# Optimization experiments

Hardware: AMD Instinct MI355X
Metric: run time of the kernel (lower is better)

## Reference

```python
import jax, jax.numpy as jnp
import numpy as np

N_NODES = 100000
N_EDGES = 1600000
IN_DIM = 512
HID = 64
OUT_DIM = 5


def _gcn_conv(x, row, col, w, W, b, n_nodes):
    """PyG GCNConv: h = x @ W; out[col] += norm * h[row]; out += b.
    norm = deg^-1/2[row] * w * deg^-1/2[col], deg from edge weights scattered on col,
    with self-loops (weight 1) already appended by caller."""
    h = x @ W  # [N, F_out]
    deg = jax.ops.segment_sum(w, col, num_segments=n_nodes)  # [N]
    dinv = jnp.where(deg > 0, jax.lax.rsqrt(deg), 0.0)
    norm = dinv[row] * w * dinv[col]  # [E']
    msg = h[row] * norm[:, None]  # [E', F_out] edge-wise gather + scale
    out = jax.ops.segment_sum(msg, col, num_segments=n_nodes)  # scatter-add
    return out + b


def setup_inputs() -> dict:
    key = jax.random.key(0)
    ks = jax.random.split(key, 10)
    x = jax.random.normal(ks[0], (N_NODES, IN_DIM), dtype=jnp.float32)
    edge_index = jax.random.randint(ks[1], (2, N_EDGES), 0, N_NODES, dtype=jnp.int32)
    edge_attr = jax.random.uniform(ks[2], (N_EDGES,), dtype=jnp.float32)
    # Glorot-ish init for params
    W1 = jax.random.normal(ks[3], (IN_DIM, HID), dtype=jnp.float32) * (1.0 / np.sqrt(IN_DIM))
    b1 = jnp.zeros((HID,), dtype=jnp.float32)
    W2 = jax.random.normal(ks[4], (HID, HID), dtype=jnp.float32) * (1.0 / np.sqrt(HID))
    b2 = jnp.zeros((HID,), dtype=jnp.float32)
    Wfc = jax.random.normal(ks[5], (HID, OUT_DIM), dtype=jnp.float32) * (1.0 / np.sqrt(HID))
    bfc = jnp.zeros((OUT_DIM,), dtype=jnp.float32)
    return {"x": x, "edge_index": edge_index, "edge_attr": edge_attr,
            "W1": W1, "b1": b1, "W2": W2, "b2": b2, "Wfc": Wfc, "bfc": bfc}


def reference(x, edge_index, edge_attr, W1, b1, W2, b2, Wfc, bfc):
    n = x.shape[0]
    loop = jnp.arange(n, dtype=edge_index.dtype)
    row = jnp.concatenate([edge_index[0], loop])  # source nodes + self-loops
    col = jnp.concatenate([edge_index[1], loop])  # target nodes + self-loops
    w = jnp.concatenate([edge_attr, jnp.ones((n,), dtype=edge_attr.dtype)])
    h = jax.nn.relu(_gcn_conv(x, row, col, w, W1, b1, n))
    # dropout(p=0.5) is identity in eval/reference mode
    h = jax.nn.relu(_gcn_conv(h, row, col, w, W2, b2, n))
    return h @ Wfc + bfc
```

## Files before the change

kernel.cpp:

```cpp
#include <hip/hip_runtime.h>

#define HID 64
#define OUTD 5
#define BCAP 16384
#define PART_CHUNK 4096

typedef __attribute__((ext_vector_type(8))) short bf16x8;
typedef __attribute__((ext_vector_type(4))) float f32x4;

__device__ inline void split_bf16(float x, short& hi, short& lo) {
    unsigned u = __float_as_uint(x);
    unsigned h = u >> 16;
    float hf = __uint_as_float(h << 16);
    float lof = x - hf;
    unsigned l = __float_as_uint(lof) >> 16;
    hi = (short)h; lo = (short)l;
}

__device__ inline ushort f2bf(float x) {
    unsigned u = __float_as_uint(x);
    u += 0x7fffu + ((u >> 16) & 1u);
    return (ushort)(u >> 16);
}
__device__ inline float bf2f(ushort b) {
    return __uint_as_float(((unsigned)b) << 16);
}

__global__ void k_prep(const float* __restrict__ W1, const float* __restrict__ W2,
                       short* __restrict__ w1hi, short* __restrict__ w1lo,
                       short* __restrict__ w2hi, short* __restrict__ w2lo,
                       int* __restrict__ gcursor, int nbuck) {
    int gid = blockIdx.x * blockDim.x + threadIdx.x;
    if (gid < nbuck) gcursor[gid] = 0;
    if (gid >= 32768 + 4096) return;
    int which = (gid >= 32768);
    int g = which ? gid - 32768 : gid;
    const float* W = which ? W2 : W1;
    short* ph = which ? w2hi : w1hi;
    short* pl = which ? w2lo : w1lo;
    int b = g & 7, lane = (g >> 3) & 63, c = (g >> 9) & 3, s = g >> 11;
    int k = s * 32 + 8 * (lane >> 4) + b;
    int j = c * 16 + (lane & 15);
    float x = W[k * 64 + j];
    short hi, lo; split_bf16(x, hi, lo);
    ph[g] = hi; pl[g] = lo;
}

template<int K>
__device__ inline void gemm_body(const float* __restrict__ A,
                                 const short* __restrict__ whi,
                                 const short* __restrict__ wlo,
                                 ushort* __restrict__ C, int M, int bid, int tid) {
    const int NS = K / 32;
    int lane = tid & 63;
    int wave = tid >> 6;
    int r0 = bid * 128 + wave * 32;

    int ar0 = r0 + (lane & 15);      if (ar0 >= M) ar0 = M - 1;
    int ar1 = r0 + 16 + (lane & 15); if (ar1 >= M) ar1 = M - 1;
    const float* pa0 = A + (size_t)ar0 * K + 8 * (lane >> 4);
    const float* pa1 = A + (size_t)ar1 * K + 8 * (lane >> 4);
    const bf16x8* bh = (const bf16x8*)whi + lane;
    const bf16x8* bl = (const bf16x8*)wlo + lane;

    f32x4 acc[2][4];
    #pragma unroll
    for (int r = 0; r < 2; r++)
        #pragma unroll
        for (int c = 0; c < 4; c++) acc[r][c] = (f32x4){0.f, 0.f, 0.f, 0.f};

    #pragma unroll
    for (int s = 0; s < NS; s++) {
        float4 x0 = *(const float4*)(pa0 + s * 32);
        float4 x1 = *(const float4*)(pa0 + s * 32 + 4);
        float4 y0 = *(const float4*)(pa1 + s * 32);
        float4 y1 = *(const float4*)(pa1 + s * 32 + 4);
        float xs[8] = {x0.x, x0.y, x0.z, x0.w, x1.x, x1.y, x1.z, x1.w};
        float ys[8] = {y0.x, y0.y, y0.z, y0.w, y1.x, y1.y, y1.z, y1.w};
        bf16x8 ah0, al0, ah1, al1;
        #pragma unroll
        for (int e = 0; e < 8; e++) {
            short h, l;
            split_bf16(xs[e], h, l); ah0[e] = h; al0[e] = l;
            split_bf16(ys[e], h, l); ah1[e] = h; al1[e] = l;
        }
        #pragma unroll
        for (int c = 0; c < 4; c++) {
            bf16x8 wh = bh[(s * 4 + c) * 64];
            bf16x8 wl = bl[(s * 4 + c) * 64];
            acc[0][c] = __builtin_amdgcn_mfma_f32_16x16x32_bf16(ah0, wh, acc[0][c], 0, 0, 0);
            acc[0][c] = __builtin_amdgcn_mfma_f32_16x16x32_bf16(ah0, wl, acc[0][c], 0, 0, 0);
            acc[0][c] = __builtin_amdgcn_mfma_f32_16x16x32_bf16(al0, wh, acc[0][c], 0, 0, 0);
            acc[1][c] = __builtin_amdgcn_mfma_f32_16x16x32_bf16(ah1, wh, acc[1][c], 0, 0, 0);
            acc[1][c] = __builtin_amdgcn_mfma_f32_16x16x32_bf16(ah1, wl, acc[1][c], 0, 0, 0);
            acc[1][c] = __builtin_amdgcn_mfma_f32_16x16x32_bf16(al1, wh, acc[1][c], 0, 0, 0);
        }
    }

    #pragma unroll
    for (int r = 0; r < 2; r++) {
        #pragma unroll
        for (int reg = 0; reg < 4; reg++) {
            int grow = r0 + r * 16 + 4 * (lane >> 4) + reg;
            if (grow < M) {
                #pragma unroll
                for (int c = 0; c < 4; c++)
                    C[(size_t)grow * 64 + c * 16 + (lane & 15)] = f2bf(acc[r][c][reg]);
            }
        }
    }
}

__global__ __launch_bounds__(256) void k_fused1(const float* __restrict__ x,
                                                const short* __restrict__ w1hi,
                                                const short* __restrict__ w1lo,
                                                ushort* __restrict__ h1, int M, int gGemm,
                                                const int* __restrict__ row,
                                                const int* __restrict__ col,
                                                const float* __restrict__ ea,
                                                int* __restrict__ gcursor,
                                                int2* __restrict__ bucket_mem,
                                                int nbuck, int E) {
    __shared__ int sh[512];
    int bid = blockIdx.x;
    int t = threadIdx.x;
    if (bid < gGemm) {
        gemm_body<512>(x, w1hi, w1lo, h1, M, bid, t);
        return;
    }
    int* hist = sh;
    int* basearr = sh + 256;
    int pb = bid - gGemm;
    int e0 = pb * PART_CHUNK;
    if (t < nbuck) hist[t] = 0;
    __syncthreads();
    int cols[PART_CHUNK / 256];
    #pragma unroll
    for (int i = 0; i < PART_CHUNK / 256; i++) {
        int e = e0 + t + i * 256;
        cols[i] = (e < E) ? col[e] : -1;
        if (cols[i] >= 0) atomicAdd(&hist[cols[i] >> 9], 1);
    }
    __syncthreads();
    if (t < nbuck) {
        basearr[t] = atomicAdd(&gcursor[t], hist[t]);
        hist[t] = 0;
    }
    __syncthreads();
    #pragma unroll
    for (int i = 0; i < PART_CHUNK / 256; i++) {
        int e = e0 + t + i * 256;
        if (e < E) {
            int c = cols[i];
            int b = c >> 9;
            int pos = basearr[b] + atomicAdd(&hist[b], 1);
            if (pos < BCAP) {
                int pack = ((c & 511) << 17) | row[e];
                bucket_mem[(size_t)b * BCAP + pos] = make_int2(pack, __float_as_int(ea[e]));
            }
        }
    }
}

__global__ __launch_bounds__(256) void k_build(const int* __restrict__ gcursor,
                                               const int2* __restrict__ bucket_mem,
                                               int2* __restrict__ edges,
                                               int2* __restrict__ nodemeta,
                                               float* __restrict__ dinv, int n) {
    __shared__ int hcnt[512];
    __shared__ int hoff[512];
    __shared__ float hdeg[512];
    __shared__ int ps[256];
    int b = blockIdx.x;
    int t = threadIdx.x;
    int cntb = gcursor[b]; if (cntb > BCAP) cntb = BCAP;
    const int2* bm = bucket_mem + (size_t)b * BCAP;

    #pragma unroll
    for (int l = t; l < 512; l += 256) { hcnt[l] = 0; hdeg[l] = 0.f; }
    __syncthreads();
    for (int i = t; i < cntb; i += 256) atomicAdd(&hcnt[bm[i].x >> 17], 1);
    __syncthreads();
    int c0 = hcnt[2 * t], c1 = hcnt[2 * t + 1];
    int q0 = (c0 + 15) & ~15, q1 = (c1 + 15) & ~15;
    ps[t] = q0 + q1;
    __syncthreads();
    for (int o = 1; o < 256; o <<= 1) {
        int v = (t >= o) ? ps[t - o] : 0;
        __syncthreads();
        ps[t] += v;
        __syncthreads();
    }
    int excl = ps[t] - (q0 + q1);
    hoff[2 * t] = excl;
    hoff[2 * t + 1] = excl + q0;
    __syncthreads();
    #pragma unroll
    for (int l = t; l < 512; l += 256) hcnt[l] = 0;
    __syncthreads();
    for (int i = t; i < cntb; i += 256) {
        int2 eM = bm[i];
        int local = eM.x >> 17;
        int src = eM.x & 0x1FFFF;
        int p = hoff[local] + atomicAdd(&hcnt[local], 1);
        edges[(size_t)b * BCAP + p] = make_int2(src, eM.y);
        atomicAdd(&hdeg[local], __int_as_float(eM.y));
    }
    __syncthreads();
    #pragma unroll
    for (int l = t; l < 512; l += 256) {
        int node = b * 512 + l;
        if (node < n) {
            int cnt = hcnt[l];
            int pc = (cnt + 15) & ~15;
            for (int p2 = cnt; p2 < pc; p2++)
                edges[(size_t)b * BCAP + hoff[l] + p2] = make_int2(node, 0);
            nodemeta[node] = make_int2(b * BCAP + hoff[l], pc);
            dinv[node] = rsqrtf(hdeg[l] + 1.0f);
        }
    }
}

__global__ void k_norm(const int2* __restrict__ nodemeta, int2* __restrict__ edges,
                       const float* __restrict__ dinv, int n) {
    int gw = (blockIdx.x * blockDim.x + threadIdx.x) >> 6;
    int lane = threadIdx.x & 63;
    if (gw >= n) return;
    int2 meta = nodemeta[gw];
    int2* seg = edges + meta.x;
    for (int i = lane; i < meta.y; i += 64) {
        int2 c = seg[i];
        c.y = __float_as_int(dinv[c.x] * __int_as_float(c.y));
        seg[i] = c;
    }
}

template<int FC>
__global__ void k_gather(const ushort* __restrict__ h, const int2* __restrict__ nodemeta,
                         const int2* __restrict__ edges, const float* __restrict__ dinv,
                         const float* __restrict__ bias, const float* __restrict__ Wfc,
                         const float* __restrict__ bfc, float* __restrict__ out, int n) {
    int gw = (blockIdx.x * blockDim.x + threadIdx.x) >> 6;
    int lane = threadIdx.x & 63;
    if (gw >= n) return;
    int2 meta = nodemeta[gw];
    int cnt = meta.y;
    const int2* seg = edges + meta.x;
    float self = bf2f(h[(size_t)gw * 64 + lane]);
    float dvc = dinv[gw];
    float acc = 0.f;

    if (cnt == 16) {
        int4 p[8];
        #pragma unroll
        for (int q = 0; q < 8; q++) p[q] = *(const int4*)(seg + 2 * q);
        float v[16];
        #pragma unroll
        for (int q = 0; q < 8; q++) {
            v[2 * q]     = bf2f(h[(size_t)p[q].x * 64 + lane]);
            v[2 * q + 1] = bf2f(h[(size_t)p[q].z * 64 + lane]);
        }
        #pragma unroll
        for (int q = 0; q < 8; q++)
            acc += __int_as_float(p[q].y) * v[2 * q] + __int_as_float(p[q].w) * v[2 * q + 1];
    } else if (cnt == 32) {
        int4 pA[8], pB[8];
        #pragma unroll
        for (int q = 0; q < 8; q++) pA[q] = *(const int4*)(seg + 2 * q);
        #pragma unroll
        for (int q = 0; q < 8; q++) pB[q] = *(const int4*)(seg + 16 + 2 * q);
        float vA[16], vB[16];
        #pragma unroll
        for (int q = 0; q < 8; q++) {
            vA[2 * q]     = bf2f(h[(size_t)pA[q].x * 64 + lane]);
            vA[2 * q + 1] = bf2f(h[(size_t)pA[q].z * 64 + lane]);
        }
        #pragma unroll
        for (int q = 0; q < 8; q++) {
            vB[2 * q]     = bf2f(h[(size_t)pB[q].x * 64 + lane]);
            vB[2 * q + 1] = bf2f(h[(size_t)pB[q].z * 64 + lane]);
        }
        #pragma unroll
        for (int q = 0; q < 8; q++)
            acc += __int_as_float(pA[q].y) * vA[2 * q] + __int_as_float(pA[q].w) * vA[2 * q + 1];
        #pragma unroll
        for (int q = 0; q < 8; q++)
            acc += __int_as_float(pB[q].y) * vB[2 * q] + __int_as_float(pB[q].w) * vB[2 * q + 1];
    } else {
        for (int i = 0; i < cnt; i += 16) {
            int4 p[8];
            #pragma unroll
            for (int q = 0; q < 8; q++) p[q] = *(const int4*)(seg + i + 2 * q);
            float v[16];
            #pragma unroll
            for (int q = 0; q < 8; q++) {
                v[2 * q]     = bf2f(h[(size_t)p[q].x * 64 + lane]);
                v[2 * q + 1] = bf2f(h[(size_t)p[q].z * 64 + lane]);
            }
            #pragma unroll
            for (int q = 0; q < 8; q++)
                acc += __int_as_float(p[q].y) * v[2 * q] + __int_as_float(p[q].w) * v[2 * q + 1];
        }
    }

    acc = dvc * acc + dvc * dvc * self + bias[lane];
    acc = fmaxf(acc, 0.f);
    if (FC == 0) {
        out[(size_t)gw * 64 + lane] = acc;
    } else {
        float res = 0.f;
        #pragma unroll
        for (int j = 0; j < OUTD; j++) {
            float p = acc * Wfc[lane * OUTD + j];
            #pragma unroll
            for (int o = 1; o < 64; o <<= 1) p += __shfl_xor(p, o);
            if (lane == j) res = p;
        }
        if (lane < OUTD) out[(size_t)gw * OUTD + lane] = res + bfc[lane];
    }
}

__global__ __launch_bounds__(256) void k_gemm2(const float* __restrict__ A,
                                               const short* __restrict__ whi,
                                               const short* __restrict__ wlo,
                                               ushort* __restrict__ C, int M) {
    gemm_body<64>(A, whi, wlo, C, M, blockIdx.x, threadIdx.x);
}

extern "C" void kernel_launch(void* const* d_in, const int* in_sizes, int n_in,
                              void* d_out, int out_size, void* d_ws, size_t ws_size,
                              hipStream_t stream) {
    const float* x   = (const float*)d_in[0];
    const int*   ei  = (const int*)d_in[1];
    const float* ea  = (const float*)d_in[2];
    const float* W1  = (const float*)d_in[3];
    const float* b1  = (const float*)d_in[4];
    const float* W2  = (const float*)d_in[5];
    const float* b2  = (const float*)d_in[6];
    const float* Wfc = (const float*)d_in[7];
    const float* bfc = (const float*)d_in[8];

    const int N = in_sizes[0] / 512;
    const int E = in_sizes[1] / 2;
    const int nbuck = (N + 511) >> 9;

    const int* row = ei;
    const int* col = ei + E;

    uintptr_t p = (uintptr_t)d_ws;
    auto carve = [&](size_t bytes) -> void* {
        void* r = (void*)p;
        p += (bytes + 255) & ~(size_t)255;
        return r;
    };
    int*    gcursor    = (int*)carve((size_t)nbuck * 4);
    float*  dinv       = (float*)carve((size_t)N * 4);
    int2*   nodemeta   = (int2*)carve((size_t)N * 8);
    int2*   bucket_mem = (int2*)carve((size_t)nbuck * BCAP * 8);
    int2*   edges      = (int2*)carve((size_t)nbuck * BCAP * 8);
    short*  w1hi       = (short*)carve(32768 * 2);
    short*  w1lo       = (short*)carve(32768 * 2);
    short*  w2hi       = (short*)carve(4096 * 2);
    short*  w2lo       = (short*)carve(4096 * 2);
    ushort* hbuf       = (ushort*)carve((size_t)N * 64 * 2);
    float*  gbuf       = (float*)carve((size_t)N * 64 * 4);
    (void)ws_size;

    const int B = 256;
    int gGemm = (N + 127) / 128;
    int gPart = (E + PART_CHUNK - 1) / PART_CHUNK;
    int gWave = (N * 64 + B - 1) / B;
    int gPrep = (32768 + 4096 + B - 1) / B;

    k_prep<<<gPrep, B, 0, stream>>>(W1, W2, w1hi, w1lo, w2hi, w2lo, gcursor, nbuck);
    k_fused1<<<gGemm + gPart, B, 0, stream>>>(x, w1hi, w1lo, hbuf, N, gGemm,
                                              row, col, ea, gcursor, bucket_mem, nbuck, E);
    k_build<<<nbuck, B, 0, stream>>>(gcursor, bucket_mem, edges, nodemeta, dinv, N);
    k_norm<<<gWave, B, 0, stream>>>(nodemeta, edges, dinv, N);
    k_gather<0><<<gWave, B, 0, stream>>>(hbuf, nodemeta, edges, dinv, b1,
                                         nullptr, nullptr, gbuf, N);
    k_gemm2<<<gGemm, B, 0, stream>>>(gbuf, w2hi, w2lo, hbuf, N);
    k_gather<1><<<gWave, B, 0, stream>>>(hbuf, nodemeta, edges, dinv, b2,
                                         Wfc, bfc, (float*)d_out, N);
}
```

Baseline: 282.6 us.

## Process two nodes per wave in gather and store layer-1 output as bf16

The gather kernel now assigns two nodes per wavefront, with each lane loading two packed bf16 features as one 32-bit word. This halves the wave count and raises bytes per load. The intermediate activation after layer 1 is stored as bf16 instead of fp32, and the second GEMM reads bf16 directly, which halves that buffer's traffic but adds rounding error on layer-1 outputs. Every node segment is padded to at least 16 entries so the unified loop can always load full 16-edge chunks, at the cost of some wasted padding work.

```diff
diff --git a/kernel.cpp b/kernel.cpp
--- a/kernel.cpp
+++ b/kernel.cpp
@@ -46,12 +46,11 @@
     ph[g] = hi; pl[g] = lo;
 }
 
-template<int K>
-__device__ inline void gemm_body(const float* __restrict__ A,
-                                 const short* __restrict__ whi,
-                                 const short* __restrict__ wlo,
-                                 ushort* __restrict__ C, int M, int bid, int tid) {
-    const int NS = K / 32;
+__device__ inline void gemm1_body(const float* __restrict__ A,
+                                  const short* __restrict__ whi,
+                                  const short* __restrict__ wlo,
+                                  ushort* __restrict__ C, int M, int bid, int tid) {
+    const int K = 512, NS = 16;
     int lane = tid & 63;
     int wave = tid >> 6;
     int r0 = bid * 128 + wave * 32;
@@ -125,7 +124,7 @@
     int bid = blockIdx.x;
     int t = threadIdx.x;
     if (bid < gGemm) {
-        gemm_body<512>(x, w1hi, w1lo, h1, M, bid, t);
+        gemm1_body(x, w1hi, w1lo, h1, M, bid, t);
         return;
     }
     int* hist = sh;
@@ -182,7 +181,8 @@
     for (int i = t; i < cntb; i += 256) atomicAdd(&hcnt[bm[i].x >> 17], 1);
     __syncthreads();
     int c0 = hcnt[2 * t], c1 = hcnt[2 * t + 1];
-    int q0 = (c0 + 15) & ~15, q1 = (c1 + 15) & ~15;
+    int q0 = (c0 + 15) & ~15; if (q0 < 16) q0 = 16;
+    int q1 = (c1 + 15) & ~15; if (q1 < 16) q1 = 16;
     ps[t] = q0 + q1;
     __syncthreads();
     for (int o = 1; o < 256; o <<= 1) {
@@ -212,7 +212,7 @@
         int node = b * 512 + l;
         if (node < n) {
             int cnt = hcnt[l];
-            int pc = (cnt + 15) & ~15;
+            int pc = (cnt + 15) & ~15; if (pc < 16) pc = 16;
             for (int p2 = cnt; p2 < pc; p2++)
                 edges[(size_t)b * BCAP + hoff[l] + p2] = make_int2(node, 0);
             nodemeta[node] = make_int2(b * BCAP + hoff[l], pc);
@@ -236,95 +236,123 @@
 }
 
 template<int FC>
-__global__ void k_gather(const ushort* __restrict__ h, const int2* __restrict__ nodemeta,
-                         const int2* __restrict__ edges, const float* __restrict__ dinv,
-                         const float* __restrict__ bias, const float* __restrict__ Wfc,
-                         const float* __restrict__ bfc, float* __restrict__ out, int n) {
+__global__ void k_gather2(const ushort* __restrict__ h, const int2* __restrict__ nodemeta,
+                          const int2* __restrict__ edges, const float* __restrict__ dinv,
+                          const float* __restrict__ bias, const float* __restrict__ Wfc,
+                          const float* __restrict__ bfc, ushort* __restrict__ outb,
+                          float* __restrict__ outf, int n) {
     int gw = (blockIdx.x * blockDim.x + threadIdx.x) >> 6;
     int lane = threadIdx.x & 63;
-    if (gw >= n) return;
-    int2 meta = nodemeta[gw];
+    int half = lane >> 5;
+    int s = lane & 31;
+    int node = gw * 2 + half;
+    bool valid = (node < n);
+    if (node >= n) node = n - 1;
+
+    int2 meta = nodemeta[node];
     int cnt = meta.y;
     const int2* seg = edges + meta.x;
-    float self = bf2f(h[(size_t)gw * 64 + lane]);
-    float dvc = dinv[gw];
-    float acc = 0.f;
-
-    if (cnt == 16) {
-        int4 p[8];
-        #pragma unroll
-        for (int q = 0; q < 8; q++) p[q] = *(const int4*)(seg + 2 * q);
-        float v[16];
+    uint self_u = *(const uint*)&h[(size_t)node * 64 + 2 * s];
+    float dvc = dinv[node];
+    int othercnt = __shfl_xor(cnt, 32);
+    int maxcnt = max(cnt, othercnt);
+
+    float acc0 = 0.f, acc1 = 0.f;
+    for (int i = 0; i < maxcnt; i += 16) {
+        int base = (i < cnt) ? i : (cnt - 16);
+        float live = (i < cnt) ? 1.f : 0.f;
+        int4 m[8];
+        #pragma unroll
+        for (int q = 0; q < 8; q++) m[q] = *(const int4*)(seg + base + 2 * q);
+        uint v[16];
         #pragma unroll
         for (int q = 0; q < 8; q++) {
-            v[2 * q]     = bf2f(h[(size_t)p[q].x * 64 + lane]);
-            v[2 * q + 1] = bf2f(h[(size_t)p[q].z * 64 + lane]);
-        }
-        #pragma unroll
-        for (int q = 0; q < 8; q++)
-            acc += __int_as_float(p[q].y) * v[2 * q] + __int_as_float(p[q].w) * v[2 * q + 1];
-    } else if (cnt == 32) {
-        int4 pA[8], pB[8];
-        #pragma unroll
-        for (int q = 0; q < 8; q++) pA[q] = *(const int4*)(seg + 2 * q);
-        #pragma unroll
-        for (int q = 0; q < 8; q++) pB[q] = *(const int4*)(seg + 16 + 2 * q);
-        float vA[16], vB[16];
+            v[2 * q]     = *(const uint*)&h[(size_t)m[q].x * 64 + 2 * s];
+            v[2 * q + 1] = *(const uint*)&h[(size_t)m[q].z * 64 + 2 * s];
+        }
         #pragma unroll
         for (int q = 0; q < 8; q++) {
-            vA[2 * q]     = bf2f(h[(size_t)pA[q].x * 64 + lane]);
-            vA[2 * q + 1] = bf2f(h[(size_t)pA[q].z * 64 + lane]);
-        }
-        #pragma unroll
-        for (int q = 0; q < 8; q++) {
-            vB[2 * q]     = bf2f(h[(size_t)pB[q].x * 64 + lane]);
-            vB[2 * q + 1] = bf2f(h[(size_t)pB[q].z * 64 + lane]);
-        }
-        #pragma unroll
-        for (int q = 0; q < 8; q++)
-            acc += __int_as_float(pA[q].y) * vA[2 * q] + __int_as_float(pA[q].w) * vA[2 * q + 1];
-        #pragma unroll
-        for (int q = 0; q < 8; q++)
-            acc += __int_as_float(pB[q].y) * vB[2 * q] + __int_as_float(pB[q].w) * vB[2 * q + 1];
+            float w0 = __int_as_float(m[q].y) * live;
+            float w1 = __int_as_float(m[q].w) * live;
+            uint va = v[2 * q], vb = v[2 * q + 1];
+            acc0 += w0 * __uint_as_float(va << 16);
+            acc1 += w0 * __uint_as_float(va & 0xffff0000u);
+            acc0 += w1 * __uint_as_float(vb << 16);
+            acc1 += w1 * __uint_as_float(vb & 0xffff0000u);
+        }
+    }
+
+    float2 bv = *(const float2*)&bias[2 * s];
+    float sf0 = __uint_as_float(self_u << 16);
+    float sf1 = __uint_as_float(self_u & 0xffff0000u);
+    float r0 = fmaxf(dvc * acc0 + dvc * dvc * sf0 + bv.x, 0.f);
+    float r1 = fmaxf(dvc * acc1 + dvc * dvc * sf1 + bv.y, 0.f);
+
+    if (FC == 0) {
+        if (valid) {
+            uint o = ((uint)f2bf(r1) << 16) | (uint)f2bf(r0);
+            *(uint*)&outb[(size_t)node * 64 + 2 * s] = o;
+        }
     } else {
-        for (int i = 0; i < cnt; i += 16) {
-            int4 p[8];
+        #pragma unroll
+        for (int j = 0; j < OUTD; j++) {
+            float p = r0 * Wfc[(2 * s) * OUTD + j] + r1 * Wfc[(2 * s + 1) * OUTD + j];
             #pragma unroll
-            for (int q = 0; q < 8; q++) p[q] = *(const int4*)(seg + i + 2 * q);
-            float v[16];
-            #pragma unroll
-            for (int q = 0; q < 8; q++) {
-                v[2 * q]     = bf2f(h[(size_t)p[q].x * 64 + lane]);
-                v[2 * q + 1] = bf2f(h[(size_t)p[q].z * 64 + lane]);
-            }
-            #pragma unroll
-            for (int q = 0; q < 8; q++)
-                acc += __int_as_float(p[q].y) * v[2 * q] + __int_as_float(p[q].w) * v[2 * q + 1];
-        }
-    }
-
-    acc = dvc * acc + dvc * dvc * self + bias[lane];
-    acc = fmaxf(acc, 0.f);
-    if (FC == 0) {
-        out[(size_t)gw * 64 + lane] = acc;
-    } else {
-        float res = 0.f;
-        #pragma unroll
-        for (int j = 0; j < OUTD; j++) {
-            float p = acc * Wfc[lane * OUTD + j];
-            #pragma unroll
-            for (int o = 1; o < 64; o <<= 1) p += __shfl_xor(p, o);
-            if (lane == j) res = p;
-        }
-        if (lane < OUTD) out[(size_t)gw * OUTD + lane] = res + bfc[lane];
-    }
-}
-
-__global__ __launch_bounds__(256) void k_gemm2(const float* __restrict__ A,
+            for (int o = 1; o <= 16; o <<= 1) p += __shfl_xor(p, o);
+            if (s == j && valid) outf[(size_t)node * OUTD + j] = p + bfc[j];
+        }
+    }
+}
+
+__global__ __launch_bounds__(256) void k_gemm2(const ushort* __restrict__ A,
                                                const short* __restrict__ whi,
                                                const short* __restrict__ wlo,
                                                ushort* __restrict__ C, int M) {
-    gemm_body<64>(A, whi, wlo, C, M, blockIdx.x, threadIdx.x);
+    int tid = threadIdx.x;
+    int lane = tid & 63;
+    int wave = tid >> 6;
+    int r0 = blockIdx.x * 128 + wave * 32;
+
+    int ar0 = r0 + (lane & 15);      if (ar0 >= M) ar0 = M - 1;
+    int ar1 = r0 + 16 + (lane & 15); if (ar1 >= M) ar1 = M - 1;
+    const ushort* pa0 = A + (size_t)ar0 * 64 + 8 * (lane >> 4);
+    const ushort* pa1 = A + (size_t)ar1 * 64 + 8 * (lane >> 4);
+    const bf16x8* bh = (const bf16x8*)whi + lane;
+    const bf16x8* bl = (const bf16x8*)wlo + lane;
+
+    f32x4 acc[2][4];
+    #pragma unroll
+    for (int r = 0; r < 2; r++)
+        #pragma unroll
+        for (int c = 0; c < 4; c++) acc[r][c] = (f32x4){0.f, 0.f, 0.f, 0.f};
+
+    #pragma unroll
+    for (int s = 0; s < 2; s++) {
+        bf16x8 a0 = *(const bf16x8*)(pa0 + s * 32);
+        bf16x8 a1 = *(const bf16x8*)(pa1 + s * 32);
+        #pragma unroll
+        for (int c = 0; c < 4; c++) {
+            bf16x8 wh = bh[(s * 4 + c) * 64];
+            bf16x8 wl = bl[(s * 4 + c) * 64];
+            acc[0][c] = __builtin_amdgcn_mfma_f32_16x16x32_bf16(a0, wh, acc[0][c], 0, 0, 0);
+            acc[0][c] = __builtin_amdgcn_mfma_f32_16x16x32_bf16(a0, wl, acc[0][c], 0, 0, 0);
+            acc[1][c] = __builtin_amdgcn_mfma_f32_16x16x32_bf16(a1, wh, acc[1][c], 0, 0, 0);
+            acc[1][c] = __builtin_amdgcn_mfma_f32_16x16x32_bf16(a1, wl, acc[1][c], 0, 0, 0);
+        }
+    }
+
+    #pragma unroll
+    for (int r = 0; r < 2; r++) {
+        #pragma unroll
+        for (int reg = 0; reg < 4; reg++) {
+            int grow = r0 + r * 16 + 4 * (lane >> 4) + reg;
+            if (grow < M) {
+                #pragma unroll
+                for (int c = 0; c < 4; c++)
+                    C[(size_t)grow * 64 + c * 16 + (lane & 15)] = f2bf(acc[r][c][reg]);
+            }
+        }
+    }
 }
 
 extern "C" void kernel_launch(void* const* d_in, const int* in_sizes, int n_in,
@@ -363,23 +391,24 @@
     short*  w2hi       = (short*)carve(4096 * 2);
     short*  w2lo       = (short*)carve(4096 * 2);
     ushort* hbuf       = (ushort*)carve((size_t)N * 64 * 2);
-    float*  gbuf       = (float*)carve((size_t)N * 64 * 4);
+    ushort* abuf       = (ushort*)carve((size_t)N * 64 * 2);
     (void)ws_size;
 
     const int B = 256;
-    int gGemm = (N + 127) / 128;
-    int gPart = (E + PART_CHUNK - 1) / PART_CHUNK;
-    int gWave = (N * 64 + B - 1) / B;
-    int gPrep = (32768 + 4096 + B - 1) / B;
+    int gGemm  = (N + 127) / 128;
+    int gPart  = (E + PART_CHUNK - 1) / PART_CHUNK;
+    int gWave  = (N * 64 + B - 1) / B;
+    int gWave2 = (((N + 1) / 2) * 64 + B - 1) / B;
+    int gPrep  = (32768 + 4096 + B - 1) / B;
 
     k_prep<<<gPrep, B, 0, stream>>>(W1, W2, w1hi, w1lo, w2hi, w2lo, gcursor, nbuck);
     k_fused1<<<gGemm + gPart, B, 0, stream>>>(x, w1hi, w1lo, hbuf, N, gGemm,
                                               row, col, ea, gcursor, bucket_mem, nbuck, E);
     k_build<<<nbuck, B, 0, stream>>>(gcursor, bucket_mem, edges, nodemeta, dinv, N);
     k_norm<<<gWave, B, 0, stream>>>(nodemeta, edges, dinv, N);
-    k_gather<0><<<gWave, B, 0, stream>>>(hbuf, nodemeta, edges, dinv, b1,
-                                         nullptr, nullptr, gbuf, N);
-    k_gemm2<<<gGemm, B, 0, stream>>>(gbuf, w2hi, w2lo, hbuf, N);
-    k_gather<1><<<gWave, B, 0, stream>>>(hbuf, nodemeta, edges, dinv, b2,
-                                         Wfc, bfc, (float*)d_out, N);
-}
+    k_gather2<0><<<gWave2, B, 0, stream>>>(hbuf, nodemeta, edges, dinv, b1,
+                                           nullptr, nullptr, abuf, nullptr, N);
+    k_gemm2<<<gGemm, B, 0, stream>>>(abuf, w2hi, w2lo, hbuf, N);
+    k_gather2<1><<<gWave2, B, 0, stream>>>(hbuf, nodemeta, edges, dinv, b2,
+                                           Wfc, bfc, nullptr, (float*)d_out, N);
+}
```

Result: faster. 245.0 us (-13.3%).
